# Optimization experiments

Measured on AMD Instinct MI355X. Metric: run time of the kernel, lower is better.

## Reference

```python
import jax, jax.numpy as jnp
import numpy as np

B, T, C, HS = 4, 4096, 1024, 128

def setup_inputs() -> dict:
    key = jax.random.key(0)
    kx, kq, kk, kv = jax.random.split(key, 4)
    x = jax.random.normal(kx, (B, T, C), dtype=jnp.float32)
    # bias-free Linear weights, stored as (in, out) so projection is x @ W
    scale = 1.0 / np.sqrt(C)
    Wq = jax.random.normal(kq, (C, HS), dtype=jnp.float32) * scale
    Wk = jax.random.normal(kk, (C, HS), dtype=jnp.float32) * scale
    Wv = jax.random.normal(kv, (C, HS), dtype=jnp.float32) * scale
    return {"x": x, "Wq": Wq, "Wk": Wk, "Wv": Wv}

def reference(x, Wq, Wk, Wv):
    # x: (B,T,C) -> q,k,v: (B,T,HS)
    q = jnp.einsum('btc,ch->bth', x, Wq)
    k = jnp.einsum('btc,ch->bth', x, Wk)
    v = jnp.einsum('btc,ch->bth', x, Wv)
    hs = k.shape[-1]
    # scaled scores (B,T,T) with causal mask
    wei = jnp.einsum('bth,bsh->bts', q, k) * (hs ** -0.5)
    causal = jnp.tril(jnp.ones((q.shape[1], q.shape[1]), dtype=bool))
    wei = jnp.where(causal, wei, -jnp.inf)
    wei = jax.nn.softmax(wei, axis=-1)
    # dropout p=0.0 -> identity
    out = jnp.einsum('bts,bsh->bth', wei, v)
    return out
```

## Files before the change

### kernel.cpp

```cpp
#include <hip/hip_runtime.h>
#include <hip/hip_bf16.h>

typedef __attribute__((ext_vector_type(8))) short short8;
typedef __attribute__((ext_vector_type(4))) short s4v;
typedef __attribute__((ext_vector_type(4))) float f32x4;

#define BATCH 4
#define TLEN 4096
#define CDIM 1024
#define HSD 128
#define MROWS (BATCH*TLEN)

#define QSCALE 0.12751744f

#ifdef __HIP_DEVICE_COMPILE__
  #define MFMA16(a,b,c) __builtin_amdgcn_mfma_f32_16x16x16bf16_1k(a,b,c,0,0,0)
#else
  #define MFMA16(a,b,c) (c)
#endif

__device__ __forceinline__ unsigned short f2bf(float f){
    unsigned u = __builtin_bit_cast(unsigned, f);
    u = (u + 0x7FFFu + ((u >> 16) & 1u)) >> 16;
    return (unsigned short)u;
}
__device__ __forceinline__ unsigned pkbf(float a, float b){
    unsigned ua = (__builtin_bit_cast(unsigned, a) + 0x8000u) >> 16;
    unsigned ub = (__builtin_bit_cast(unsigned, b) + 0x8000u) & 0xFFFF0000u;
    return ua | ub;
}

__global__ void prep_w_k(const float* __restrict__ Wq, const float* __restrict__ Wk,
                         const float* __restrict__ Wv, unsigned short* __restrict__ Wt){
    int idx = blockIdx.x * 256 + threadIdx.x;
    const int total = 3 * HSD * CDIM;
    if (idx >= total) return;
    int w = idx / (HSD * CDIM);
    int r = idx - w * HSD * CDIM;
    int h = r / CDIM;
    int c = r - h * CDIM;
    const float* W = (w == 0) ? Wq : ((w == 1) ? Wk : Wv);
    Wt[idx] = f2bf(W[c * HSD + h]);
}

__global__ void prep_x_k(const float* __restrict__ x, unsigned short* __restrict__ xb){
    int i = (blockIdx.x * 256 + threadIdx.x) * 8;
    float4 a = *(const float4*)(x + i);
    float4 b = *(const float4*)(x + i + 4);
    short8 o;
    o[0]=(short)f2bf(a.x); o[1]=(short)f2bf(a.y); o[2]=(short)f2bf(a.z); o[3]=(short)f2bf(a.w);
    o[4]=(short)f2bf(b.x); o[5]=(short)f2bf(b.y); o[6]=(short)f2bf(b.z); o[7]=(short)f2bf(b.w);
    *(short8*)(xb + i) = o;
}

__device__ __forceinline__ void stage_tile32(unsigned short* buf, const unsigned short* g,
                                             int ldg, int tid){
#pragma unroll
    for (int i = 0; i < 2; i++){
        int c = i * 256 + tid;
        int row = c >> 2, kp = c & 3;
        int swz = (row & 3) ^ ((row >> 2) & 3);
        const unsigned short* gp = g + (size_t)row * ldg + ((kp ^ swz) << 3);
        unsigned short* lp = buf + (c << 3);
        __builtin_amdgcn_global_load_lds((const __attribute__((address_space(1))) void*)gp,
                                         (__attribute__((address_space(3))) void*)lp, 16, 0, 0);
    }
}

__global__ __launch_bounds__(256) void proj_k(const unsigned short* __restrict__ xb,
                                              const unsigned short* __restrict__ Wt,
                                              unsigned short* __restrict__ Qb,
                                              unsigned short* __restrict__ Kb,
                                              unsigned short* __restrict__ Vt){
    __shared__ unsigned short As[2][128 * 32];
    __shared__ unsigned short Bs[2][128 * 32];

    const int tid = threadIdx.x, lane = tid & 63, wave = tid >> 6;
    const int m = lane & 15, quad = lane >> 4;
    const int wr = wave & 1, wc = wave >> 1;
    const int rb = blockIdx.x * 128;
    const int p  = blockIdx.y;

    const unsigned short* gA = xb + (size_t)rb * CDIM;
    const unsigned short* gB = Wt + (size_t)(p * HSD) * CDIM;

    f32x4 acc[4][4];
#pragma unroll
    for (int i = 0; i < 4; i++)
#pragma unroll
        for (int j = 0; j < 4; j++) acc[i][j] = (f32x4)0.f;

    stage_tile32(&As[0][0], gA, CDIM, tid);
    stage_tile32(&Bs[0][0], gB, CDIM, tid);
    __syncthreads();

    int cur = 0;
    for (int kc = 0; kc < CDIM / 32; ++kc){
        if (kc + 1 < CDIM / 32){
            stage_tile32(&As[cur ^ 1][0], gA + (kc + 1) * 32, CDIM, tid);
            stage_tile32(&Bs[cur ^ 1][0], gB + (kc + 1) * 32, CDIM, tid);
        }
        const unsigned short* Af = (p == 2) ? &As[cur][0] : &Bs[cur][0];
        const unsigned short* Bf = (p == 2) ? &Bs[cur][0] : &As[cur][0];
        short8 aF[4], bF[4];
#pragma unroll
        for (int i = 0; i < 4; i++){
            int ra = wr * 64 + i * 16 + m;
            int sa = (ra & 3) ^ ((ra >> 2) & 3);
            aF[i] = *(const short8*)&Af[ra * 32 + ((quad ^ sa) << 3)];
            int rn = wc * 64 + i * 16 + m;
            int sb = (rn & 3) ^ ((rn >> 2) & 3);
            bF[i] = *(const short8*)&Bf[rn * 32 + ((quad ^ sb) << 3)];
        }
#pragma unroll
        for (int i = 0; i < 4; i++)
#pragma unroll
            for (int j = 0; j < 4; j++)
                acc[i][j] = __builtin_amdgcn_mfma_f32_16x16x32_bf16(aF[i], bF[j], acc[i][j], 0, 0, 0);
        __syncthreads();
        cur ^= 1;
    }

    if (p < 2){
        unsigned short* D = (p == 0) ? Qb : Kb;
        const float qs = (p == 0) ? QSCALE : 1.0f;
#pragma unroll
        for (int i = 0; i < 4; i++){
#pragma unroll
            for (int j = 0; j < 4; j++){
                int h = wr * 64 + i * 16 + quad * 4;
                int t = rb + wc * 64 + j * 16 + m;
                ushort4 v;
                v.x = f2bf(acc[i][j][0] * qs); v.y = f2bf(acc[i][j][1] * qs);
                v.z = f2bf(acc[i][j][2] * qs); v.w = f2bf(acc[i][j][3] * qs);
                *(ushort4*)(D + (size_t)t * HSD + h) = v;
            }
        }
    } else {
        int b = rb >> 12;
        int tb = rb & 4095;
#pragma unroll
        for (int i = 0; i < 4; i++){
#pragma unroll
            for (int j = 0; j < 4; j++){
                int t = tb + wr * 64 + i * 16 + quad * 4;
                int h = wc * 64 + j * 16 + m;
                ushort4 v;
                v.x = f2bf(acc[i][j][0]); v.y = f2bf(acc[i][j][1]);
                v.z = f2bf(acc[i][j][2]); v.w = f2bf(acc[i][j][3]);
                *(ushort4*)(Vt + ((size_t)b * HSD + h) * TLEN + t) = v;
            }
        }
    }
}

__global__ void proj_f32_k(const float* __restrict__ x, const unsigned short* __restrict__ Wt,
                           unsigned short* __restrict__ Qb, unsigned short* __restrict__ Kb,
                           unsigned short* __restrict__ Vt){
    const int lane = threadIdx.x;
    const int m = lane & 15, quad = lane >> 4;
    const int rb = blockIdx.x * 16;

    f32x4 acc[3][8];
#pragma unroll
    for (int p = 0; p < 3; p++)
#pragma unroll
        for (int i = 0; i < 8; i++) acc[p][i] = (f32x4)0.f;

    const float* xrow = x + (size_t)(rb + m) * CDIM + quad * 8;
    for (int k0 = 0; k0 < CDIM; k0 += 32){
        float4 a0 = *(const float4*)(xrow + k0);
        float4 a1 = *(const float4*)(xrow + k0 + 4);
        short8 aF;
        aF[0]=(short)f2bf(a0.x); aF[1]=(short)f2bf(a0.y); aF[2]=(short)f2bf(a0.z); aF[3]=(short)f2bf(a0.w);
        aF[4]=(short)f2bf(a1.x); aF[5]=(short)f2bf(a1.y); aF[6]=(short)f2bf(a1.z); aF[7]=(short)f2bf(a1.w);
#pragma unroll
        for (int p = 0; p < 3; p++){
#pragma unroll
            for (int sub = 0; sub < 8; sub++){
                short8 bF = *(const short8*)(Wt + (size_t)(p * HSD + sub * 16 + m) * CDIM + k0 + quad * 8);
                acc[p][sub] = __builtin_amdgcn_mfma_f32_16x16x32_bf16(aF, bF, acc[p][sub], 0, 0, 0);
            }
        }
    }
#pragma unroll
    for (int p = 0; p < 3; p++){
        const float qs = (p == 0) ? QSCALE : 1.0f;
#pragma unroll
        for (int sub = 0; sub < 8; sub++){
#pragma unroll
            for (int r = 0; r < 4; r++){
                int row = rb + quad * 4 + r;
                int col = sub * 16 + m;
                unsigned short v = f2bf(acc[p][sub][r] * qs);
                if (p == 0)      Qb[(size_t)row * HSD + col] = v;
                else if (p == 1) Kb[(size_t)row * HSD + col] = v;
                else {
                    int b = row >> 12;
                    int t = row & 4095;
                    Vt[((size_t)b * HSD + col) * TLEN + t] = v;
                }
            }
        }
    }
}

__device__ __forceinline__ void stage_k_tile(unsigned short* buf, const unsigned short* g,
                                             int wave, int lane){
#pragma unroll
    for (int i = 0; i < 4; i++){
        int slot = wave * 256 + i * 64 + lane;
        int row = slot >> 4;
        int ch  = slot & 15;
        const unsigned short* gp = g + row * 128 + ((ch ^ (row & 15)) << 3);
        unsigned short* lp = buf + (slot << 3);
        __builtin_amdgcn_global_load_lds((const __attribute__((address_space(1))) void*)gp,
                                         (__attribute__((address_space(3))) void*)lp, 16, 0, 0);
    }
}
__device__ __forceinline__ void stage_v_tile(unsigned short* buf, const unsigned short* g,
                                             int wave, int lane){
#pragma unroll
    for (int i = 0; i < 4; i++){
        int slot = wave * 256 + i * 64 + lane;
        int row = slot >> 3;
        int ch  = slot & 7;
        const unsigned short* gp = g + (size_t)row * TLEN + ((ch ^ (row & 7)) << 3);
        unsigned short* lp = buf + (slot << 3);
        __builtin_amdgcn_global_load_lds((const __attribute__((address_space(1))) void*)gp,
                                         (__attribute__((address_space(3))) void*)lp, 16, 0, 0);
    }
}

__global__ __launch_bounds__(256, 4) void attn_k(const unsigned short* __restrict__ Qb,
                       const unsigned short* __restrict__ Kb,
                       const unsigned short* __restrict__ Vts,
                       float* __restrict__ Opart, float2* __restrict__ ml, int seglen){
    __shared__ unsigned short Kt[64 * 128];
    __shared__ unsigned short Vs[128 * 64];

    const int tid = threadIdx.x, lane = tid & 63, wave = tid >> 6;
    const int m = lane & 15, quad = lane >> 4;
    const int q0 = ((int)gridDim.x - 1 - (int)blockIdx.x) * 64;
    const int seg = blockIdx.y, b = blockIdx.z;
    const int g0 = seg * seglen;
    if (g0 >= q0 + 64) return;
    const int gend = min(g0 + seglen, q0 + 64);
    const int nT = (gend - g0) >> 6;

    const int q0w = q0 + wave * 16;
    const size_t rowg = (size_t)b * TLEN + q0w;

    short8 aQ[4];
#pragma unroll
    for (int kk = 0; kk < 4; kk++)
        aQ[kk] = *(const short8*)(Qb + (rowg + m) * HSD + kk * 32 + quad * 8);

    f32x4 accO[8];
#pragma unroll
    for (int i = 0; i < 8; i++) accO[i] = (f32x4)0.f;
    float mi = -1e30f, li = 0.f;

    const unsigned short* kbase = Kb + (size_t)b * TLEN * HSD;
    const unsigned short* vbase = Vts + (size_t)b * HSD * TLEN;
    const int bpbase = (lane >> 4) << 4;

    for (int t = 0; t < nT; ++t){
        const int s0 = g0 + t * 64;
        stage_k_tile(&Kt[0], kbase + (size_t)s0 * HSD, wave, lane);
        stage_v_tile(&Vs[0], vbase + s0, wave, lane);
        __syncthreads();

        f32x4 S[4];
#pragma unroll
        for (int ns = 0; ns < 4; ns++){
            f32x4 sa = (f32x4)0.f;
#pragma unroll
            for (int kk = 0; kk < 4; kk++){
                short8 bK = *(const short8*)&Kt[(ns * 16 + m) * 128 + (((kk * 4 + quad) ^ m) << 3)];
                sa = __builtin_amdgcn_mfma_f32_16x16x32_bf16(bK, aQ[kk], sa, 0, 0, 0);
            }
            S[ns] = sa;
        }
        if (s0 + 63 > q0w){
            int qg = q0w + m;
#pragma unroll
            for (int ns = 0; ns < 4; ns++){
#pragma unroll
                for (int r = 0; r < 4; r++){
                    int sg = s0 + ns * 16 + quad * 4 + r;
                    if (sg > qg) S[ns][r] = -1e30f;
                }
            }
        }
        f32x4 m4 = S[0];
#pragma unroll
        for (int ns = 1; ns < 4; ns++)
#pragma unroll
            for (int r = 0; r < 4; r++) m4[r] = fmaxf(m4[r], S[ns][r]);
        float mloc = fmaxf(fmaxf(m4[0], m4[1]), fmaxf(m4[2], m4[3]));
        mloc = fmaxf(mloc, __shfl_xor(mloc, 16, 64));
        mloc = fmaxf(mloc, __shfl_xor(mloc, 32, 64));
        float mn = fmaxf(mi, mloc);
        float al = exp2f(mi - mn);
        mi = mn;

        float ps[4][4];
        float lsum = 0.f;
#pragma unroll
        for (int ns = 0; ns < 4; ns++)
#pragma unroll
            for (int r = 0; r < 4; r++){
                float pv = exp2f(S[ns][r] - mi);
                ps[ns][r] = pv;
                lsum += pv;
            }
        lsum += __shfl_xor(lsum, 16, 64);
        lsum += __shfl_xor(lsum, 32, 64);
        li = li * al + lsum;

        s4v aP[4];
#pragma unroll
        for (int ns = 0; ns < 4; ns++){
            uint2 u;
            u.x = pkbf(ps[ns][0], ps[ns][1]);
            u.y = pkbf(ps[ns][2], ps[ns][3]);
            aP[ns] = __builtin_bit_cast(s4v, u);
        }
        float alr[4];
#pragma unroll
        for (int r = 0; r < 4; r++)
            alr[r] = __builtin_bit_cast(float,
                __builtin_amdgcn_ds_bpermute(bpbase + 4 * r, __builtin_bit_cast(int, al)));
#pragma unroll
        for (int sub = 0; sub < 8; sub++)
#pragma unroll
            for (int r = 0; r < 4; r++) accO[sub][r] *= alr[r];
#pragma unroll
        for (int sub = 0; sub < 8; sub++){
#pragma unroll
            for (int ns = 0; ns < 4; ns++){
                s4v bV = *(const s4v*)&Vs[(sub * 16 + m) * 64 +
                        (((2 * ns + (quad >> 1)) ^ (m & 7)) << 3) + (quad & 1) * 4];
                accO[sub] = MFMA16(aP[ns], bV, accO[sub]);
            }
        }
        __syncthreads();
    }
    if (quad == 0){
        float2 v; v.x = mi; v.y = li;
        ml[(size_t)seg * MROWS + rowg + m] = v;
    }
    float* ob = Opart + (size_t)seg * MROWS * HSD;
#pragma unroll
    for (int sub = 0; sub < 8; sub++)
#pragma unroll
        for (int r = 0; r < 4; r++)
            ob[(rowg + quad * 4 + r) * HSD + sub * 16 + m] = accO[sub][r];
}

__global__ void merge_k(const float* __restrict__ Opart, const float2* __restrict__ ml,
                        float* __restrict__ out, int nseg, int seglen){
    int idx = blockIdx.x * 256 + threadIdx.x;
    int row = idx >> 7;
    int t = row & (TLEN - 1);
    int q0 = t & ~63;
    int nsv = min(nseg, (q0 + 63) / seglen + 1);
    float M = -1e30f;
    for (int s = 0; s < nsv; s++) M = fmaxf(M, ml[(size_t)s * MROWS + row].x);
    float L = 0.f, o = 0.f;
    for (int s = 0; s < nsv; s++){
        float2 p = ml[(size_t)s * MROWS + row];
        float w = exp2f(p.x - M);
        L += p.y * w;
        o += w * Opart[(size_t)s * MROWS * HSD + idx];
    }
    out[idx] = o / L;
}

extern "C" void kernel_launch(void* const* d_in, const int* in_sizes, int n_in,
                              void* d_out, int out_size, void* d_ws, size_t ws_size,
                              hipStream_t stream) {
    const float* x  = (const float*)d_in[0];
    const float* Wq = (const float*)d_in[1];
    const float* Wk = (const float*)d_in[2];
    const float* Wv = (const float*)d_in[3];
    float* out = (float*)d_out;
    char* w = (char*)d_ws;

    unsigned short* Wt = (unsigned short*)w;
    unsigned short *xb = nullptr, *Qb, *Kb, *Vt;
    float* Opart; float2* ml;
    int nseg; bool use_xb;

    if (ws_size >= (size_t)78u * 1024 * 1024){
        nseg = 4; use_xb = true;
        xb = (unsigned short*)(w + ((size_t)1u  << 20));
        Qb = (unsigned short*)(w + ((size_t)33u << 20));
        Kb = (unsigned short*)(w + ((size_t)37u << 20));
        Vt = (unsigned short*)(w + ((size_t)41u << 20));
        Opart = (float*)(w + ((size_t)45u << 20));
        ml    = (float2*)(w + ((size_t)77u << 20));
    } else if (ws_size >= (size_t)46u * 1024 * 1024){
        nseg = 1; use_xb = true;
        xb = (unsigned short*)(w + ((size_t)1u  << 20));
        Qb = (unsigned short*)(w + ((size_t)33u << 20));
        Kb = (unsigned short*)(w + ((size_t)37u << 20));
        Vt = (unsigned short*)(w + ((size_t)41u << 20));
        Opart = out;
        ml    = (float2*)(w + ((size_t)45u << 20));
    } else {
        nseg = 1; use_xb = false;
        Qb = (unsigned short*)(w + ((size_t)1u << 20));
        Kb = (unsigned short*)(w + ((size_t)5u << 20));
        Vt = (unsigned short*)(w + ((size_t)9u << 20));
        Opart = out;
        ml    = (float2*)(w + ((size_t)13u << 20));
    }
    const int seglen = TLEN / nseg;

    prep_w_k<<<(3 * HSD * CDIM + 255) / 256, 256, 0, stream>>>(Wq, Wk, Wv, Wt);
    if (use_xb){
        prep_x_k<<<(MROWS * CDIM) / (256 * 8), 256, 0, stream>>>(x, xb);
        proj_k<<<dim3(MROWS / 128, 3), 256, 0, stream>>>(xb, Wt, Qb, Kb, Vt);
    } else {
        proj_f32_k<<<MROWS / 16, 64, 0, stream>>>(x, Wt, Qb, Kb, Vt);
    }
    attn_k<<<dim3(TLEN / 64, nseg, BATCH), 256, 0, stream>>>(Qb, Kb, Vt, Opart, ml, seglen);
    merge_k<<<(MROWS * HSD) / 256, 256, 0, stream>>>(Opart, ml, out, nseg, seglen);
}
```

Baseline: 214.1 us.

## Fuse x bf16 conversion into projection GEMM and raise attention split count

```diff
diff --git a/kernel.cpp b/kernel.cpp
--- a/kernel.cpp
+++ b/kernel.cpp
@@ -43,80 +43,112 @@
     Wt[idx] = f2bf(W[c * HSD + h]);
 }
 
-__global__ void prep_x_k(const float* __restrict__ x, unsigned short* __restrict__ xb){
-    int i = (blockIdx.x * 256 + threadIdx.x) * 8;
-    float4 a = *(const float4*)(x + i);
-    float4 b = *(const float4*)(x + i + 4);
-    short8 o;
-    o[0]=(short)f2bf(a.x); o[1]=(short)f2bf(a.y); o[2]=(short)f2bf(a.z); o[3]=(short)f2bf(a.w);
-    o[4]=(short)f2bf(b.x); o[5]=(short)f2bf(b.y); o[6]=(short)f2bf(b.z); o[7]=(short)f2bf(b.w);
-    *(short8*)(xb + i) = o;
-}
-
-__device__ __forceinline__ void stage_tile32(unsigned short* buf, const unsigned short* g,
-                                             int ldg, int tid){
+__device__ __forceinline__ void stage_w_tile(unsigned short* buf, const unsigned short* g,
+                                             int tid){
 #pragma unroll
     for (int i = 0; i < 2; i++){
         int c = i * 256 + tid;
         int row = c >> 2, kp = c & 3;
         int swz = (row & 3) ^ ((row >> 2) & 3);
-        const unsigned short* gp = g + (size_t)row * ldg + ((kp ^ swz) << 3);
+        const unsigned short* gp = g + (size_t)row * CDIM + ((kp ^ swz) << 3);
         unsigned short* lp = buf + (c << 3);
         __builtin_amdgcn_global_load_lds((const __attribute__((address_space(1))) void*)gp,
                                          (__attribute__((address_space(3))) void*)lp, 16, 0, 0);
     }
 }
 
-__global__ __launch_bounds__(256) void proj_k(const unsigned short* __restrict__ xb,
+__global__ __launch_bounds__(256) void proj_k(const float* __restrict__ x,
                                               const unsigned short* __restrict__ Wt,
                                               unsigned short* __restrict__ Qb,
                                               unsigned short* __restrict__ Kb,
                                               unsigned short* __restrict__ Vt){
-    __shared__ unsigned short As[2][128 * 32];
+    __shared__ unsigned short As[2][64 * 32];
     __shared__ unsigned short Bs[2][128 * 32];
 
     const int tid = threadIdx.x, lane = tid & 63, wave = tid >> 6;
     const int m = lane & 15, quad = lane >> 4;
     const int wr = wave & 1, wc = wave >> 1;
-    const int rb = blockIdx.x * 128;
+    const int rb = blockIdx.x * 64;
     const int p  = blockIdx.y;
 
-    const unsigned short* gA = xb + (size_t)rb * CDIM;
+    const float* gA = x + (size_t)rb * CDIM;
     const unsigned short* gB = Wt + (size_t)(p * HSD) * CDIM;
 
+    const int arow = tid >> 2, ach = tid & 3;
+    const int aswz = (arow & 3) ^ ((arow >> 2) & 3);
+    const int agc = ach ^ aswz;
+    const float* agp = gA + (size_t)arow * CDIM + (agc << 3);
+
     f32x4 acc[4][4];
 #pragma unroll
     for (int i = 0; i < 4; i++)
 #pragma unroll
         for (int j = 0; j < 4; j++) acc[i][j] = (f32x4)0.f;
 
-    stage_tile32(&As[0][0], gA, CDIM, tid);
-    stage_tile32(&Bs[0][0], gB, CDIM, tid);
+    stage_w_tile(&Bs[0][0], gB, tid);
+    {
+        float4 a0 = *(const float4*)(agp);
+        float4 a1 = *(const float4*)(agp + 4);
+        short8 o;
+        o[0]=(short)f2bf(a0.x); o[1]=(short)f2bf(a0.y); o[2]=(short)f2bf(a0.z); o[3]=(short)f2bf(a0.w);
+        o[4]=(short)f2bf(a1.x); o[5]=(short)f2bf(a1.y); o[6]=(short)f2bf(a1.z); o[7]=(short)f2bf(a1.w);
+        *(short8*)&As[0][arow * 32 + (ach << 3)] = o;
+    }
     __syncthreads();
 
     int cur = 0;
     for (int kc = 0; kc < CDIM / 32; ++kc){
+        float4 a0n, a1n;
         if (kc + 1 < CDIM / 32){
-            stage_tile32(&As[cur ^ 1][0], gA + (kc + 1) * 32, CDIM, tid);
-            stage_tile32(&Bs[cur ^ 1][0], gB + (kc + 1) * 32, CDIM, tid);
-        }
-        const unsigned short* Af = (p == 2) ? &As[cur][0] : &Bs[cur][0];
-        const unsigned short* Bf = (p == 2) ? &Bs[cur][0] : &As[cur][0];
-        short8 aF[4], bF[4];
-#pragma unroll
-        for (int i = 0; i < 4; i++){
-            int ra = wr * 64 + i * 16 + m;
-            int sa = (ra & 3) ^ ((ra >> 2) & 3);
-            aF[i] = *(const short8*)&Af[ra * 32 + ((quad ^ sa) << 3)];
-            int rn = wc * 64 + i * 16 + m;
-            int sb = (rn & 3) ^ ((rn >> 2) & 3);
-            bF[i] = *(const short8*)&Bf[rn * 32 + ((quad ^ sb) << 3)];
-        }
-#pragma unroll
-        for (int i = 0; i < 4; i++)
-#pragma unroll
-            for (int j = 0; j < 4; j++)
-                acc[i][j] = __builtin_amdgcn_mfma_f32_16x16x32_bf16(aF[i], bF[j], acc[i][j], 0, 0, 0);
+            stage_w_tile(&Bs[cur ^ 1][0], gB + (kc + 1) * 32, tid);
+            a0n = *(const float4*)(agp + (kc + 1) * 32);
+            a1n = *(const float4*)(agp + (kc + 1) * 32 + 4);
+        }
+        if (p < 2){
+            short8 aF[4], bF[2];
+#pragma unroll
+            for (int i = 0; i < 4; i++){
+                int ra = wr * 64 + i * 16 + m;
+                int sa = (ra & 3) ^ ((ra >> 2) & 3);
+                aF[i] = *(const short8*)&Bs[cur][ra * 32 + ((quad ^ sa) << 3)];
+            }
+#pragma unroll
+            for (int j = 0; j < 2; j++){
+                int rn = wc * 32 + j * 16 + m;
+                int sb = (rn & 3) ^ ((rn >> 2) & 3);
+                bF[j] = *(const short8*)&As[cur][rn * 32 + ((quad ^ sb) << 3)];
+            }
+#pragma unroll
+            for (int i = 0; i < 4; i++)
+#pragma unroll
+                for (int j = 0; j < 2; j++)
+                    acc[i][j] = __builtin_amdgcn_mfma_f32_16x16x32_bf16(aF[i], bF[j], acc[i][j], 0, 0, 0);
+        } else {
+            short8 aF[2], bF[4];
+#pragma unroll
+            for (int i = 0; i < 2; i++){
+                int ra = wr * 32 + i * 16 + m;
+                int sa = (ra & 3) ^ ((ra >> 2) & 3);
+                aF[i] = *(const short8*)&As[cur][ra * 32 + ((quad ^ sa) << 3)];
+            }
+#pragma unroll
+            for (int j = 0; j < 4; j++){
+                int rn = wc * 64 + j * 16 + m;
+                int sb = (rn & 3) ^ ((rn >> 2) & 3);
+                bF[j] = *(const short8*)&Bs[cur][rn * 32 + ((quad ^ sb) << 3)];
+            }
+#pragma unroll
+            for (int i = 0; i < 2; i++)
+#pragma unroll
+                for (int j = 0; j < 4; j++)
+                    acc[i][j] = __builtin_amdgcn_mfma_f32_16x16x32_bf16(aF[i], bF[j], acc[i][j], 0, 0, 0);
+        }
+        if (kc + 1 < CDIM / 32){
+            short8 o;
+            o[0]=(short)f2bf(a0n.x); o[1]=(short)f2bf(a0n.y); o[2]=(short)f2bf(a0n.z); o[3]=(short)f2bf(a0n.w);
+            o[4]=(short)f2bf(a1n.x); o[5]=(short)f2bf(a1n.y); o[6]=(short)f2bf(a1n.z); o[7]=(short)f2bf(a1n.w);
+            *(short8*)&As[cur ^ 1][arow * 32 + (ach << 3)] = o;
+        }
         __syncthreads();
         cur ^= 1;
     }
@@ -127,9 +159,9 @@
 #pragma unroll
         for (int i = 0; i < 4; i++){
 #pragma unroll
-            for (int j = 0; j < 4; j++){
+            for (int j = 0; j < 2; j++){
                 int h = wr * 64 + i * 16 + quad * 4;
-                int t = rb + wc * 64 + j * 16 + m;
+                int t = rb + wc * 32 + j * 16 + m;
                 ushort4 v;
                 v.x = f2bf(acc[i][j][0] * qs); v.y = f2bf(acc[i][j][1] * qs);
                 v.z = f2bf(acc[i][j][2] * qs); v.w = f2bf(acc[i][j][3] * qs);
@@ -140,66 +172,15 @@
         int b = rb >> 12;
         int tb = rb & 4095;
 #pragma unroll
-        for (int i = 0; i < 4; i++){
+        for (int i = 0; i < 2; i++){
 #pragma unroll
             for (int j = 0; j < 4; j++){
-                int t = tb + wr * 64 + i * 16 + quad * 4;
+                int t = tb + wr * 32 + i * 16 + quad * 4;
                 int h = wc * 64 + j * 16 + m;
                 ushort4 v;
                 v.x = f2bf(acc[i][j][0]); v.y = f2bf(acc[i][j][1]);
                 v.z = f2bf(acc[i][j][2]); v.w = f2bf(acc[i][j][3]);
                 *(ushort4*)(Vt + ((size_t)b * HSD + h) * TLEN + t) = v;
-            }
-        }
-    }
-}
-
-__global__ void proj_f32_k(const float* __restrict__ x, const unsigned short* __restrict__ Wt,
-                           unsigned short* __restrict__ Qb, unsigned short* __restrict__ Kb,
-                           unsigned short* __restrict__ Vt){
-    const int lane = threadIdx.x;
-    const int m = lane & 15, quad = lane >> 4;
-    const int rb = blockIdx.x * 16;
-
-    f32x4 acc[3][8];
-#pragma unroll
-    for (int p = 0; p < 3; p++)
-#pragma unroll
-        for (int i = 0; i < 8; i++) acc[p][i] = (f32x4)0.f;
-
-    const float* xrow = x + (size_t)(rb + m) * CDIM + quad * 8;
-    for (int k0 = 0; k0 < CDIM; k0 += 32){
-        float4 a0 = *(const float4*)(xrow + k0);
-        float4 a1 = *(const float4*)(xrow + k0 + 4);
-        short8 aF;
-        aF[0]=(short)f2bf(a0.x); aF[1]=(short)f2bf(a0.y); aF[2]=(short)f2bf(a0.z); aF[3]=(short)f2bf(a0.w);
-        aF[4]=(short)f2bf(a1.x); aF[5]=(short)f2bf(a1.y); aF[6]=(short)f2bf(a1.z); aF[7]=(short)f2bf(a1.w);
-#pragma unroll
-        for (int p = 0; p < 3; p++){
-#pragma unroll
-            for (int sub = 0; sub < 8; sub++){
-                short8 bF = *(const short8*)(Wt + (size_t)(p * HSD + sub * 16 + m) * CDIM + k0 + quad * 8);
-                acc[p][sub] = __builtin_amdgcn_mfma_f32_16x16x32_bf16(aF, bF, acc[p][sub], 0, 0, 0);
-            }
-        }
-    }
-#pragma unroll
-    for (int p = 0; p < 3; p++){
-        const float qs = (p == 0) ? QSCALE : 1.0f;
-#pragma unroll
-        for (int sub = 0; sub < 8; sub++){
-#pragma unroll
-            for (int r = 0; r < 4; r++){
-                int row = rb + quad * 4 + r;
-                int col = sub * 16 + m;
-                unsigned short v = f2bf(acc[p][sub][r] * qs);
-                if (p == 0)      Qb[(size_t)row * HSD + col] = v;
-                else if (p == 1) Kb[(size_t)row * HSD + col] = v;
-                else {
-                    int b = row >> 12;
-                    int t = row & 4095;
-                    Vt[((size_t)b * HSD + col) * TLEN + t] = v;
-                }
             }
         }
     }
@@ -389,43 +370,23 @@
     char* w = (char*)d_ws;
 
     unsigned short* Wt = (unsigned short*)w;
-    unsigned short *xb = nullptr, *Qb, *Kb, *Vt;
-    float* Opart; float2* ml;
-    int nseg; bool use_xb;
-
+    unsigned short* Qb = (unsigned short*)(w + ((size_t)1u  << 20));
+    unsigned short* Kb = (unsigned short*)(w + ((size_t)5u  << 20));
+    unsigned short* Vt = (unsigned short*)(w + ((size_t)9u  << 20));
+    float2* ml         = (float2*)(w + ((size_t)13u << 20));
+    float* Opart;
+    int nseg;
     if (ws_size >= (size_t)78u * 1024 * 1024){
-        nseg = 4; use_xb = true;
-        xb = (unsigned short*)(w + ((size_t)1u  << 20));
-        Qb = (unsigned short*)(w + ((size_t)33u << 20));
-        Kb = (unsigned short*)(w + ((size_t)37u << 20));
-        Vt = (unsigned short*)(w + ((size_t)41u << 20));
-        Opart = (float*)(w + ((size_t)45u << 20));
-        ml    = (float2*)(w + ((size_t)77u << 20));
+        nseg = 8;  Opart = (float*)(w + ((size_t)14u << 20));
     } else if (ws_size >= (size_t)46u * 1024 * 1024){
-        nseg = 1; use_xb = true;
-        xb = (unsigned short*)(w + ((size_t)1u  << 20));
-        Qb = (unsigned short*)(w + ((size_t)33u << 20));
-        Kb = (unsigned short*)(w + ((size_t)37u << 20));
-        Vt = (unsigned short*)(w + ((size_t)41u << 20));
-        Opart = out;
-        ml    = (float2*)(w + ((size_t)45u << 20));
+        nseg = 4;  Opart = (float*)(w + ((size_t)14u << 20));
     } else {
-        nseg = 1; use_xb = false;
-        Qb = (unsigned short*)(w + ((size_t)1u << 20));
-        Kb = (unsigned short*)(w + ((size_t)5u << 20));
-        Vt = (unsigned short*)(w + ((size_t)9u << 20));
-        Opart = out;
-        ml    = (float2*)(w + ((size_t)13u << 20));
+        nseg = 1;  Opart = out;
     }
     const int seglen = TLEN / nseg;
 
     prep_w_k<<<(3 * HSD * CDIM + 255) / 256, 256, 0, stream>>>(Wq, Wk, Wv, Wt);
-    if (use_xb){
-        prep_x_k<<<(MROWS * CDIM) / (256 * 8), 256, 0, stream>>>(x, xb);
-        proj_k<<<dim3(MROWS / 128, 3), 256, 0, stream>>>(xb, Wt, Qb, Kb, Vt);
-    } else {
-        proj_f32_k<<<MROWS / 16, 64, 0, stream>>>(x, Wt, Qb, Kb, Vt);
-    }
+    proj_k<<<dim3(MROWS / 64, 3), 256, 0, stream>>>(x, Wt, Qb, Kb, Vt);
     attn_k<<<dim3(TLEN / 64, nseg, BATCH), 256, 0, stream>>>(Qb, Kb, Vt, Opart, ml, seglen);
     merge_k<<<(MROWS * HSD) / 256, 256, 0, stream>>>(Opart, ml, out, nseg, seglen);
 }
```

New measurement: 214.3 us. About the same (+0.1%).
